# Optimization experiments

Measured on AMD Instinct MI355X. Metric: run time of the kernel, lower is better.

The kernel has to match this reference:

```python
import jax, jax.numpy as jnp
import numpy as np

HEADS = 8
DIM_HEAD = 64
SCALE = DIM_HEAD ** -0.5
QUERY_DIM = 512
CTX_DIM = 64
INNER = HEADS * DIM_HEAD  # 512
GATE_HID = 32


def setup_inputs() -> dict:
    key = jax.random.key(0)
    ks = jax.random.split(key, 11)
    B, N, M = 4, 2048, 2048
    s = lambda fan: 1.0 / np.sqrt(fan)
    return {
        "x": jax.random.normal(ks[0], (B, N, QUERY_DIM), dtype=jnp.float32),
        "context": jax.random.normal(ks[1], (B, M, CTX_DIM), dtype=jnp.float32),
        "Wq": jax.random.normal(ks[2], (QUERY_DIM, INNER), dtype=jnp.float32) * s(QUERY_DIM),
        "Wk": jax.random.normal(ks[3], (CTX_DIM, INNER), dtype=jnp.float32) * s(CTX_DIM),
        "Wv": jax.random.normal(ks[4], (CTX_DIM, INNER), dtype=jnp.float32) * s(CTX_DIM),
        "W1": jax.random.normal(ks[5], (CTX_DIM, GATE_HID), dtype=jnp.float32) * s(CTX_DIM),
        "b1": jnp.zeros((GATE_HID,), dtype=jnp.float32),
        "W2": jax.random.normal(ks[6], (GATE_HID, 1), dtype=jnp.float32) * s(GATE_HID),
        "b2": jnp.zeros((1,), dtype=jnp.float32),
        "Wo": jax.random.normal(ks[7], (INNER, QUERY_DIM), dtype=jnp.float32) * s(INNER),
        "bo": jnp.zeros((QUERY_DIM,), dtype=jnp.float32),
    }


def reference(x, context, Wq, Wk, Wv, W1, b1, W2, b2, Wo, bo):
    B, N, _ = x.shape
    M = context.shape[1]
    # visual reliability gate: sigmoid(relu(ctx @ W1 + b1) @ W2 + b2) -> [B, M, 1]
    gate = jax.nn.sigmoid(jax.nn.relu(context @ W1 + b1) @ W2 + b2)
    ctx = context * gate
    # projections
    q = (x @ Wq).reshape(B, N, HEADS, DIM_HEAD).transpose(0, 2, 1, 3)    # [B,H,N,D]
    k = (ctx @ Wk).reshape(B, M, HEADS, DIM_HEAD).transpose(0, 2, 1, 3)  # [B,H,M,D]
    v = (ctx @ Wv).reshape(B, M, HEADS, DIM_HEAD).transpose(0, 2, 1, 3)  # [B,H,M,D]
    # scaled dot-product attention (full score matrix, as in source)
    sim = jnp.einsum('bhid,bhjd->bhij', q, k) * SCALE
    attn = jax.nn.softmax(sim, axis=-1)
    out = jnp.einsum('bhij,bhjd->bhid', attn, v)
    out = out.transpose(0, 2, 1, 3).reshape(B, N, INNER)
    return out @ Wo + bo
```

## Files before the change

### kernel.cpp

```cpp
#include <hip/hip_runtime.h>

typedef unsigned short u16;
typedef unsigned int u32;
using frag16 = __attribute__((ext_vector_type(8))) short;
using facc   = __attribute__((ext_vector_type(4))) float;
using facc16 = __attribute__((ext_vector_type(16))) float;

#define DEV static __device__ __forceinline__

DEV u16 f2bf(float f) {
  union { float f; unsigned u; } v; v.f = f;
  unsigned r = v.u + 0x7fffu + ((v.u >> 16) & 1u);
  return (u16)(r >> 16);
}
DEV unsigned fbits(float f) {
  union { float f; unsigned u; } v; v.f = f;
  return v.u;
}
DEV unsigned pkbf(float lo, float hi) {
  return __builtin_amdgcn_perm(fbits(hi) + 0x8000u, fbits(lo) + 0x8000u, 0x07060302u);
}
DEV unsigned pkbf_t(float lo, float hi) {
  return __builtin_amdgcn_perm(fbits(hi), fbits(lo), 0x07060302u);
}
DEV void gld16(const u16* g, u16* l) {
  __builtin_amdgcn_global_load_lds(
      (__attribute__((address_space(1))) unsigned int*)(g),
      (__attribute__((address_space(3))) unsigned int*)(l), 16, 0, 0);
}

__global__ __launch_bounds__(256) void prep_gate_kernel(const float4* __restrict__ x,
    const float* __restrict__ Wq, const float* __restrict__ Wk,
    const float* __restrict__ Wv, const float* __restrict__ Wo,
    const float* __restrict__ ctx, const float* __restrict__ W1,
    const float* __restrict__ b1, const float* __restrict__ W2,
    const float* __restrict__ b2,
    u16* __restrict__ xb, u16* __restrict__ WqT, u16* __restrict__ WkT,
    u16* __restrict__ WvT, u16* __restrict__ WoT, u16* __restrict__ gctx) {
  int bid = blockIdx.x;
  if (bid < 4096) {
    int id = bid * 256 + threadIdx.x;
    float4 v = x[id];
    ushort4 o;
    o.x = f2bf(v.x); o.y = f2bf(v.y); o.z = f2bf(v.z); o.w = f2bf(v.w);
    *(ushort4*)(xb + (size_t)id * 4) = o;
  } else if (bid < 4240) {
    int job = bid - 4096;
    const float* W; u16* WT; int K, tile;
    if (job < 64)      { W = Wq; WT = WqT; K = 512; tile = job; }
    else if (job < 72) { W = Wk; WT = WkT; K = 64;  tile = job - 64; }
    else if (job < 80) { W = Wv; WT = WvT; K = 64;  tile = job - 72; }
    else               { W = Wo; WT = WoT; K = 512; tile = job - 80; }
    int tilesK = K >> 6;
    int tr = tile % tilesK, tc = tile / tilesK;
    __shared__ float tl[64][65];
    int c = threadIdx.x & 63, r4 = threadIdx.x >> 6;
    #pragma unroll
    for (int it = 0; it < 16; ++it) {
      int kk = it * 4 + r4;
      tl[kk][c] = W[(size_t)(tr * 64 + kk) * 512 + tc * 64 + c];
    }
    __syncthreads();
    #pragma unroll
    for (int it = 0; it < 16; ++it) {
      int nn = it * 4 + r4;
      WT[(size_t)(tc * 64 + nn) * K + tr * 64 + c] = f2bf(tl[c][nn]);
    }
  } else {
    int wave = threadIdx.x >> 6, lane = threadIdx.x & 63;
    int row = (bid - 4240) * 4 + wave;
    __shared__ float sc[4][64];
    float cv = ctx[(size_t)row * 64 + lane];
    sc[wave][lane] = cv;
    __syncthreads();
    float h = 0.f;
    if (lane < 32) {
      h = b1[lane];
      #pragma unroll
      for (int i = 0; i < 64; ++i) h += sc[wave][i] * W1[i * 32 + lane];
      h = fmaxf(h, 0.f) * W2[lane];
    }
    #pragma unroll
    for (int off = 32; off; off >>= 1) h += __shfl_xor(h, off);
    float g = 1.f / (1.f + __expf(-(h + b2[0])));
    gctx[(size_t)row * 64 + lane] = f2bf(cv * g);
  }
}

template<int MODE>
DEV void gemm128_body(const u16* __restrict__ A, const u16* __restrict__ BT,
                      void* __restrict__ Cp, const float* __restrict__ bias,
                      int m0, int n0, float scale,
                      u16* As0, u16* As1, u16* Bs0, u16* Bs1) {
  const int K = 512, N = 512;
  const int lane = threadIdx.x & 63, wave = threadIdx.x >> 6;
  const int quad = lane >> 4, l16 = lane & 15;
  const int wr = wave >> 1, wc = wave & 1;

  const u16* gA = A + (size_t)(m0 + wave * 32 + (lane >> 2)) * K + (lane & 3) * 8;
  const u16* gB = BT + (size_t)(n0 + wave * 16 + (lane >> 2)) * K + (lane & 3) * 8;

  facc acc[4][2] = {};

  for (int k0 = 0; k0 < K; k0 += 64) {
    if (k0) __syncthreads();
    gld16(gA + k0,           As0 + wave * 1024);
    gld16(gA + 16 * K + k0,  As0 + wave * 1024 + 512);
    gld16(gA + k0 + 32,          As1 + wave * 1024);
    gld16(gA + 16 * K + k0 + 32, As1 + wave * 1024 + 512);
    gld16(gB + k0,      Bs0 + wave * 512);
    gld16(gB + k0 + 32, Bs1 + wave * 512);
    __syncthreads();

    #pragma unroll
    for (int hh = 0; hh < 2; ++hh) {
      const u16* Ah = hh ? As1 : As0;
      const u16* Bh = hh ? Bs1 : Bs0;
      frag16 af[4], bf[2];
      #pragma unroll
      for (int rt = 0; rt < 4; ++rt)
        af[rt] = *(const frag16*)(Ah + (wr * 64 + rt * 16 + l16) * 32 + quad * 8);
      #pragma unroll
      for (int ct = 0; ct < 2; ++ct)
        bf[ct] = *(const frag16*)(Bh + (wc * 32 + ct * 16 + l16) * 32 + quad * 8);
      #pragma unroll
      for (int rt = 0; rt < 4; ++rt)
        #pragma unroll
        for (int ct = 0; ct < 2; ++ct)
          acc[rt][ct] = __builtin_amdgcn_mfma_f32_16x16x32_bf16(af[rt], bf[ct], acc[rt][ct], 0, 0, 0);
    }
  }

  #pragma unroll
  for (int rt = 0; rt < 4; ++rt) {
    #pragma unroll
    for (int ct = 0; ct < 2; ++ct) {
      int col = n0 + wc * 32 + ct * 16 + l16;
      int r0g = m0 + wr * 64 + rt * 16 + quad * 4;
      if (MODE == 0) {
        u16* C = (u16*)Cp;
        #pragma unroll
        for (int r = 0; r < 4; ++r)
          C[(size_t)(r0g + r) * N + col] = f2bf(acc[rt][ct][r] * scale);
      } else {
        float* C = (float*)Cp;
        float bv = bias[col];
        #pragma unroll
        for (int r = 0; r < 4; ++r)
          C[(size_t)(r0g + r) * N + col] = acc[rt][ct][r] + bv;
      }
    }
  }
}

__global__ __launch_bounds__(256) void proj_kernel(const u16* __restrict__ xb,
    const u16* __restrict__ WqT, u16* __restrict__ qb,
    const u16* __restrict__ gctx, const u16* __restrict__ BkT,
    const u16* __restrict__ BvT, u16* __restrict__ Kp, u16* __restrict__ Vp) {
  __shared__ __align__(16) u16 As0[128 * 32], As1[128 * 32];
  __shared__ __align__(16) u16 Bs0[64 * 32], Bs1[64 * 32];
  int bid = blockIdx.x;
  if (bid < 512) {
    int n0 = (bid & 7) * 64, m0 = (bid >> 3) * 128;
    gemm128_body<0>(xb, WqT, qb, nullptr, m0, n0,
                    0.125f * 1.4426950408889634f, As0, As1, Bs0, Bs1);
    return;
  }
  bid -= 512;
  const int Kd = 64;
  int lane = threadIdx.x & 63, wave = threadIdx.x >> 6;
  int quad = lane >> 4, l16 = lane & 15;
  int wr = wave >> 1, wc = wave & 1;
  int rowBase = (bid >> 3) * 64 + wr * 32;
  int colBase = (bid & 7) * 64 + wc * 32;
  facc ak[2][2] = {}, av[2][2] = {};
  const u16* a0 = gctx + (size_t)(rowBase + l16) * Kd + quad * 8;
  const u16* a1 = a0 + (size_t)16 * Kd;
  const u16* bk0 = BkT + (size_t)(colBase + l16) * Kd + quad * 8;
  const u16* bk1 = bk0 + (size_t)16 * Kd;
  const u16* bv0 = BvT + (size_t)(colBase + l16) * Kd + quad * 8;
  const u16* bv1 = bv0 + (size_t)16 * Kd;
  #pragma unroll
  for (int kk = 0; kk < Kd; kk += 32) {
    frag16 af0 = *(const frag16*)(a0 + kk);
    frag16 af1 = *(const frag16*)(a1 + kk);
    frag16 k0 = *(const frag16*)(bk0 + kk);
    frag16 k1 = *(const frag16*)(bk1 + kk);
    frag16 v0 = *(const frag16*)(bv0 + kk);
    frag16 v1 = *(const frag16*)(bv1 + kk);
    ak[0][0] = __builtin_amdgcn_mfma_f32_16x16x32_bf16(af0, k0, ak[0][0], 0, 0, 0);
    ak[0][1] = __builtin_amdgcn_mfma_f32_16x16x32_bf16(af0, k1, ak[0][1], 0, 0, 0);
    ak[1][0] = __builtin_amdgcn_mfma_f32_16x16x32_bf16(af1, k0, ak[1][0], 0, 0, 0);
    ak[1][1] = __builtin_amdgcn_mfma_f32_16x16x32_bf16(af1, k1, ak[1][1], 0, 0, 0);
    av[0][0] = __builtin_amdgcn_mfma_f32_16x16x32_bf16(af0, v0, av[0][0], 0, 0, 0);
    av[0][1] = __builtin_amdgcn_mfma_f32_16x16x32_bf16(af0, v1, av[0][1], 0, 0, 0);
    av[1][0] = __builtin_amdgcn_mfma_f32_16x16x32_bf16(af1, v0, av[1][0], 0, 0, 0);
    av[1][1] = __builtin_amdgcn_mfma_f32_16x16x32_bf16(af1, v1, av[1][1], 0, 0, 0);
  }
  #pragma unroll
  for (int rt = 0; rt < 2; ++rt) {
    #pragma unroll
    for (int ct = 0; ct < 2; ++ct) {
      int col = colBase + ct * 16 + l16;
      int r0g = rowBase + rt * 16 + quad * 4;
      int hh = col >> 6, d = col & 63;
      int b = r0g >> 11;
      #pragma unroll
      for (int r = 0; r < 4; ++r) {
        int m = (r0g + r) & 2047;
        size_t addr = ((((size_t)(b * 8 + hh) * 64 + (m >> 5)) * 4 + (d >> 4)) * 64
                       + ((d >> 3) & 1) * 32 + (m & 31)) * 8 + (d & 7);
        Kp[addr] = f2bf(ak[rt][ct][r]);
      }
      int m = r0g & 2047;
      size_t addr = ((((size_t)(b * 8 + hh) * 64 + (m >> 5)) * 4
                      + ((m >> 4) & 1) * 2 + (d >> 5)) * 64
                     + ((m >> 3) & 1) * 32 + (d & 31)) * 8 + (m & 7);
      ushort4 o;
      o.x = f2bf(av[rt][ct][0]); o.y = f2bf(av[rt][ct][1]);
      o.z = f2bf(av[rt][ct][2]); o.w = f2bf(av[rt][ct][3]);
      *(ushort4*)(Vp + addr) = o;
    }
  }
}

__global__ __launch_bounds__(256, 2) void attn_kernel(
    const u16* __restrict__ qb, const u16* __restrict__ Kp,
    const u16* __restrict__ Vp, u16* __restrict__ ob) {
  const int lane = threadIdx.x & 63, wave = threadIdx.x >> 6;
  const int l32 = lane & 31;
  const int hi = lane >> 5;
  const int bid = blockIdx.x;
  const int bh = bid & 31;
  const int qblk = bid >> 5;
  const int b = bh >> 3, h = bh & 7;
  const int q0 = (qblk * 4 + wave) * 32;
  const int rowg = b * 2048 + q0 + l32;

  __shared__ __align__(16) u16 sK[3][2][2048], sV[3][2][2048];

  const u16* qp = qb + (size_t)rowg * 512 + h * 64 + hi * 8;
  frag16 qf0 = *(const frag16*)(qp);
  frag16 qf1 = *(const frag16*)(qp + 16);
  frag16 qf2 = *(const frag16*)(qp + 32);
  frag16 qf3 = *(const frag16*)(qp + 48);

  frag16 ones;
  #pragma unroll
  for (int i = 0; i < 8; ++i) ones[i] = (short)0x3F80;

  facc16 O0 = {}, O1 = {}, Lacc = {};

  const size_t ts = 2048;
  const u16* kpb = Kp + (size_t)(bh * 64) * ts + wave * 512 + lane * 8;
  const u16* vpb = Vp + (size_t)(bh * 64) * ts + wave * 512 + lane * 8;

  auto STAGE = [&](int g, int buf) {
    const size_t t2 = (size_t)(2 * g) * ts;
    gld16(kpb + t2,      &sK[buf][0][0] + wave * 512);
    gld16(kpb + t2 + ts, &sK[buf][1][0] + wave * 512);
    gld16(vpb + t2,      &sV[buf][0][0] + wave * 512);
    gld16(vpb + t2 + ts, &sV[buf][1][0] + wave * 512);
  };

  STAGE(0, 0);
  STAGE(1, 1);

  int p = 0;
  #pragma unroll 1
  for (int g = 0; g < 32; ++g) {
    if (g < 31) {
      asm volatile("s_waitcnt vmcnt(4) lgkmcnt(0)" ::: "memory");
    } else {
      asm volatile("s_waitcnt vmcnt(0) lgkmcnt(0)" ::: "memory");
    }
    __builtin_amdgcn_s_barrier();

    const u16* kbase = &sK[p][0][0];
    const u16* vbase = &sV[p][0][0];

    frag16 kfa[4], kfb[4];
    #pragma unroll
    for (int i = 0; i < 4; ++i) {
      kfa[i] = *(const frag16*)(kbase + i * 512 + lane * 8);
      kfb[i] = *(const frag16*)(kbase + 2048 + i * 512 + lane * 8);
    }

    if (g + 2 < 32) {
      int ps = p + 2; if (ps >= 3) ps -= 3;
      STAGE(g + 2, ps);
    }

    facc16 Sa = {}, Sb = {};
    Sa = __builtin_amdgcn_mfma_f32_32x32x16_bf16(kfa[0], qf0, Sa, 0, 0, 0);
    Sb = __builtin_amdgcn_mfma_f32_32x32x16_bf16(kfb[0], qf0, Sb, 0, 0, 0);
    Sa = __builtin_amdgcn_mfma_f32_32x32x16_bf16(kfa[1], qf1, Sa, 0, 0, 0);
    Sb = __builtin_amdgcn_mfma_f32_32x32x16_bf16(kfb[1], qf1, Sb, 0, 0, 0);
    Sa = __builtin_amdgcn_mfma_f32_32x32x16_bf16(kfa[2], qf2, Sa, 0, 0, 0);
    Sb = __builtin_amdgcn_mfma_f32_32x32x16_bf16(kfb[2], qf2, Sb, 0, 0, 0);
    Sa = __builtin_amdgcn_mfma_f32_32x32x16_bf16(kfa[3], qf3, Sa, 0, 0, 0);
    Sb = __builtin_amdgcn_mfma_f32_32x32x16_bf16(kfb[3], qf3, Sb, 0, 0, 0);

    float ea[16], eb[16];
    #pragma unroll
    for (int r = 0; r < 16; ++r) { ea[r] = __builtin_amdgcn_exp2f(Sa[r]);
                                   eb[r] = __builtin_amdgcn_exp2f(Sb[r]); }

    unsigned pua[2][4], pub[2][4];
    #pragma unroll
    for (int c = 0; c < 2; ++c) {
      {
        const float* ee = ea + c * 8;
        unsigned L0 = pkbf_t(ee[0], ee[1]);
        unsigned L1 = pkbf_t(ee[2], ee[3]);
        unsigned H0 = pkbf_t(ee[4], ee[5]);
        unsigned H1 = pkbf_t(ee[6], ee[7]);
        unsigned Y0 = hi ? L0 : H0;
        unsigned Y1 = hi ? L1 : H1;
        unsigned X0 = (unsigned)__shfl_xor((int)Y0, 32);
        unsigned X1 = (unsigned)__shfl_xor((int)Y1, 32);
        pua[c][0] = hi ? X0 : L0;
        pua[c][1] = hi ? X1 : L1;
        pua[c][2] = hi ? H0 : X0;
        pua[c][3] = hi ? H1 : X1;
      }
      {
        const float* ee = eb + c * 8;
        unsigned L0 = pkbf_t(ee[0], ee[1]);
        unsigned L1 = pkbf_t(ee[2], ee[3]);
        unsigned H0 = pkbf_t(ee[4], ee[5]);
        unsigned H1 = pkbf_t(ee[6], ee[7]);
        unsigned Y0 = hi ? L0 : H0;
        unsigned Y1 = hi ? L1 : H1;
        unsigned X0 = (unsigned)__shfl_xor((int)Y0, 32);
        unsigned X1 = (unsigned)__shfl_xor((int)Y1, 32);
        pub[c][0] = hi ? X0 : L0;
        pub[c][1] = hi ? X1 : L1;
        pub[c][2] = hi ? H0 : X0;
        pub[c][3] = hi ? H1 : X1;
      }
    }
    frag16 Pa0 = *(frag16*)&pua[0][0];
    frag16 Pa1 = *(frag16*)&pua[1][0];
    frag16 Pb0 = *(frag16*)&pub[0][0];
    frag16 Pb1 = *(frag16*)&pub[1][0];

    Lacc = __builtin_amdgcn_mfma_f32_32x32x16_bf16(ones, Pa0, Lacc, 0, 0, 0);
    Lacc = __builtin_amdgcn_mfma_f32_32x32x16_bf16(ones, Pa1, Lacc, 0, 0, 0);
    Lacc = __builtin_amdgcn_mfma_f32_32x32x16_bf16(ones, Pb0, Lacc, 0, 0, 0);
    Lacc = __builtin_amdgcn_mfma_f32_32x32x16_bf16(ones, Pb1, Lacc, 0, 0, 0);

    frag16 vfa[4], vfb[4];
    #pragma unroll
    for (int i = 0; i < 4; ++i) {
      vfa[i] = *(const frag16*)(vbase + i * 512 + lane * 8);
      vfb[i] = *(const frag16*)(vbase + 2048 + i * 512 + lane * 8);
    }

    O0 = __builtin_amdgcn_mfma_f32_32x32x16_bf16(vfa[0], Pa0, O0, 0, 0, 0);
    O1 = __builtin_amdgcn_mfma_f32_32x32x16_bf16(vfa[1], Pa0, O1, 0, 0, 0);
    O0 = __builtin_amdgcn_mfma_f32_32x32x16_bf16(vfa[2], Pa1, O0, 0, 0, 0);
    O1 = __builtin_amdgcn_mfma_f32_32x32x16_bf16(vfa[3], Pa1, O1, 0, 0, 0);
    O0 = __builtin_amdgcn_mfma_f32_32x32x16_bf16(vfb[0], Pb0, O0, 0, 0, 0);
    O1 = __builtin_amdgcn_mfma_f32_32x32x16_bf16(vfb[1], Pb0, O1, 0, 0, 0);
    O0 = __builtin_amdgcn_mfma_f32_32x32x16_bf16(vfb[2], Pb1, O0, 0, 0, 0);
    O1 = __builtin_amdgcn_mfma_f32_32x32x16_bf16(vfb[3], Pb1, O1, 0, 0, 0);

    ++p; if (p == 3) p = 0;
  }

  float rinv = 1.0f / Lacc[0];

  u16* op = ob + (size_t)rowg * 512 + h * 64;
  #pragma unroll
  for (int dt = 0; dt < 2; ++dt) {
    #pragma unroll
    for (int rq = 0; rq < 4; ++rq) {
      float v0e, v1e, v2e, v3e;
      if (dt == 0) { v0e = O0[rq*4]; v1e = O0[rq*4+1]; v2e = O0[rq*4+2]; v3e = O0[rq*4+3]; }
      else         { v0e = O1[rq*4]; v1e = O1[rq*4+1]; v2e = O1[rq*4+2]; v3e = O1[rq*4+3]; }
      uint2 pk;
      pk.x = pkbf(v0e * rinv, v1e * rinv);
      pk.y = pkbf(v2e * rinv, v3e * rinv);
      int d0 = dt * 32 + 8 * rq + 4 * hi;
      *(uint2*)(op + d0) = pk;
    }
  }
}

__global__ __launch_bounds__(256) void gemm_out(const u16* __restrict__ A,
    const u16* __restrict__ BT, float* __restrict__ C,
    const float* __restrict__ bias) {
  __shared__ __align__(16) u16 As0[128 * 32], As1[128 * 32];
  __shared__ __align__(16) u16 Bs0[64 * 32], Bs1[64 * 32];
  int n0 = (blockIdx.x & 7) * 64, m0 = (blockIdx.x >> 3) * 128;
  gemm128_body<2>(A, BT, C, bias, m0, n0, 1.f, As0, As1, Bs0, Bs1);
}

extern "C" void kernel_launch(void* const* d_in, const int* in_sizes, int n_in,
                              void* d_out, int out_size, void* d_ws, size_t ws_size,
                              hipStream_t stream) {
  const float* x   = (const float*)d_in[0];
  const float* ctx = (const float*)d_in[1];
  const float* Wq  = (const float*)d_in[2];
  const float* Wk  = (const float*)d_in[3];
  const float* Wv  = (const float*)d_in[4];
  const float* W1  = (const float*)d_in[5];
  const float* b1  = (const float*)d_in[6];
  const float* W2  = (const float*)d_in[7];
  const float* b2  = (const float*)d_in[8];
  const float* Wo  = (const float*)d_in[9];
  const float* bo  = (const float*)d_in[10];
  float* out = (float*)d_out;

  char* ws = (char*)d_ws;
  size_t off = 0;
  auto alloc = [&](size_t bytes) {
    char* p = ws + off;
    off += (bytes + 255) & ~(size_t)255;
    return p;
  };
  u16* xb    = (u16*)alloc(8192ull * 512 * 2);
  u16* qb    = (u16*)alloc(8192ull * 512 * 2);
  u16* Kp    = (u16*)alloc(8192ull * 512 * 2);
  u16* Vp    = (u16*)alloc(8192ull * 512 * 2);
  u16* ob    = (u16*)alloc(8192ull * 512 * 2);
  u16* gctx  = (u16*)alloc(8192ull * 64 * 2);
  u16* WqT   = (u16*)alloc(512ull * 512 * 2);
  u16* WkT   = (u16*)alloc(512ull * 64 * 2);
  u16* WvT   = (u16*)alloc(512ull * 64 * 2);
  u16* WoT   = (u16*)alloc(512ull * 512 * 2);

  prep_gate_kernel<<<6288, 256, 0, stream>>>((const float4*)x, Wq, Wk, Wv, Wo,
                                             ctx, W1, b1, W2, b2,
                                             xb, WqT, WkT, WvT, WoT, gctx);
  proj_kernel<<<1536, 256, 0, stream>>>(xb, WqT, qb, gctx, WkT, WvT, Kp, Vp);
  attn_kernel<<<512, 256, 0, stream>>>(qb, Kp, Vp, ob);
  gemm_out<<<512, 256, 0, stream>>>(ob, WoT, out, bo);
}
```

Measured before the change: 168.5 us.

## Split attention keys across wave pairs and merge partial results in LDS

Each block now handles 64 queries. Two waves per query tile each process half of the key positions, and their partial O and row sums are combined through shared memory at the end. The grid doubles to 1024 blocks, launch bounds target 4 blocks per CU, and the K/V pipeline drops from triple to double buffering with a __syncthreads per iteration. This raises parallelism and occupancy but loads K/V tiles once per two query tiles instead of four, adds a reduction step, and gives the pipeline less prefetch depth.

```diff
diff --git a/kernel.cpp b/kernel.cpp
--- a/kernel.cpp
+++ b/kernel.cpp
@@ -224,20 +224,22 @@
   }
 }
 
-__global__ __launch_bounds__(256, 2) void attn_kernel(
+__global__ __launch_bounds__(256, 4) void attn_kernel(
     const u16* __restrict__ qb, const u16* __restrict__ Kp,
     const u16* __restrict__ Vp, u16* __restrict__ ob) {
   const int lane = threadIdx.x & 63, wave = threadIdx.x >> 6;
+  const int wq = wave & 1;
+  const int ws = wave >> 1;
   const int l32 = lane & 31;
   const int hi = lane >> 5;
   const int bid = blockIdx.x;
   const int bh = bid & 31;
-  const int qblk = bid >> 5;
+  const int qpair = bid >> 5;
   const int b = bh >> 3, h = bh & 7;
-  const int q0 = (qblk * 4 + wave) * 32;
+  const int q0 = qpair * 64 + wq * 32;
   const int rowg = b * 2048 + q0 + l32;
 
-  __shared__ __align__(16) u16 sK[3][2][2048], sV[3][2][2048];
+  __shared__ __align__(16) u16 sK[2][2][2048], sV[2][2][2048];
 
   const u16* qp = qb + (size_t)rowg * 512 + h * 64 + hi * 8;
   frag16 qf0 = *(const frag16*)(qp);
@@ -252,138 +254,113 @@
   facc16 O0 = {}, O1 = {}, Lacc = {};
 
   const size_t ts = 2048;
-  const u16* kpb = Kp + (size_t)(bh * 64) * ts + wave * 512 + lane * 8;
-  const u16* vpb = Vp + (size_t)(bh * 64) * ts + wave * 512 + lane * 8;
+  const u16* kpb = Kp + (size_t)(bh * 64 + ws * 32) * ts + wq * 1024 + lane * 8;
+  const u16* vpb = Vp + (size_t)(bh * 64 + ws * 32) * ts + wq * 1024 + lane * 8;
 
   auto STAGE = [&](int g, int buf) {
-    const size_t t2 = (size_t)(2 * g) * ts;
-    gld16(kpb + t2,      &sK[buf][0][0] + wave * 512);
-    gld16(kpb + t2 + ts, &sK[buf][1][0] + wave * 512);
-    gld16(vpb + t2,      &sV[buf][0][0] + wave * 512);
-    gld16(vpb + t2 + ts, &sV[buf][1][0] + wave * 512);
+    const size_t off = (size_t)g * ts;
+    gld16(kpb + off,       &sK[buf][ws][0] + wq * 1024);
+    gld16(kpb + off + 512, &sK[buf][ws][0] + wq * 1024 + 512);
+    gld16(vpb + off,       &sV[buf][ws][0] + wq * 1024);
+    gld16(vpb + off + 512, &sV[buf][ws][0] + wq * 1024 + 512);
   };
 
   STAGE(0, 0);
-  STAGE(1, 1);
 
   int p = 0;
   #pragma unroll 1
   for (int g = 0; g < 32; ++g) {
-    if (g < 31) {
-      asm volatile("s_waitcnt vmcnt(4) lgkmcnt(0)" ::: "memory");
-    } else {
-      asm volatile("s_waitcnt vmcnt(0) lgkmcnt(0)" ::: "memory");
-    }
-    __builtin_amdgcn_s_barrier();
-
-    const u16* kbase = &sK[p][0][0];
-    const u16* vbase = &sV[p][0][0];
-
-    frag16 kfa[4], kfb[4];
-    #pragma unroll
-    for (int i = 0; i < 4; ++i) {
-      kfa[i] = *(const frag16*)(kbase + i * 512 + lane * 8);
-      kfb[i] = *(const frag16*)(kbase + 2048 + i * 512 + lane * 8);
-    }
-
-    if (g + 2 < 32) {
-      int ps = p + 2; if (ps >= 3) ps -= 3;
-      STAGE(g + 2, ps);
-    }
-
-    facc16 Sa = {}, Sb = {};
-    Sa = __builtin_amdgcn_mfma_f32_32x32x16_bf16(kfa[0], qf0, Sa, 0, 0, 0);
-    Sb = __builtin_amdgcn_mfma_f32_32x32x16_bf16(kfb[0], qf0, Sb, 0, 0, 0);
-    Sa = __builtin_amdgcn_mfma_f32_32x32x16_bf16(kfa[1], qf1, Sa, 0, 0, 0);
-    Sb = __builtin_amdgcn_mfma_f32_32x32x16_bf16(kfb[1], qf1, Sb, 0, 0, 0);
-    Sa = __builtin_amdgcn_mfma_f32_32x32x16_bf16(kfa[2], qf2, Sa, 0, 0, 0);
-    Sb = __builtin_amdgcn_mfma_f32_32x32x16_bf16(kfb[2], qf2, Sb, 0, 0, 0);
-    Sa = __builtin_amdgcn_mfma_f32_32x32x16_bf16(kfa[3], qf3, Sa, 0, 0, 0);
-    Sb = __builtin_amdgcn_mfma_f32_32x32x16_bf16(kfb[3], qf3, Sb, 0, 0, 0);
-
-    float ea[16], eb[16];
-    #pragma unroll
-    for (int r = 0; r < 16; ++r) { ea[r] = __builtin_amdgcn_exp2f(Sa[r]);
-                                   eb[r] = __builtin_amdgcn_exp2f(Sb[r]); }
-
-    unsigned pua[2][4], pub[2][4];
+    __syncthreads();
+    if (g + 1 < 32) STAGE(g + 1, p ^ 1);
+
+    const u16* kbase = &sK[p][ws][0];
+    const u16* vbase = &sV[p][ws][0];
+
+    frag16 kf0 = *(const frag16*)(kbase + 0 * 512 + lane * 8);
+    frag16 kf1 = *(const frag16*)(kbase + 1 * 512 + lane * 8);
+    frag16 kf2 = *(const frag16*)(kbase + 2 * 512 + lane * 8);
+    frag16 kf3 = *(const frag16*)(kbase + 3 * 512 + lane * 8);
+
+    facc16 Sa = {};
+    Sa = __builtin_amdgcn_mfma_f32_32x32x16_bf16(kf0, qf0, Sa, 0, 0, 0);
+    Sa = __builtin_amdgcn_mfma_f32_32x32x16_bf16(kf1, qf1, Sa, 0, 0, 0);
+    Sa = __builtin_amdgcn_mfma_f32_32x32x16_bf16(kf2, qf2, Sa, 0, 0, 0);
+    Sa = __builtin_amdgcn_mfma_f32_32x32x16_bf16(kf3, qf3, Sa, 0, 0, 0);
+
+    float ea[16];
+    #pragma unroll
+    for (int r = 0; r < 16; ++r) ea[r] = __builtin_amdgcn_exp2f(Sa[r]);
+
+    unsigned pua[2][4];
     #pragma unroll
     for (int c = 0; c < 2; ++c) {
-      {
-        const float* ee = ea + c * 8;
-        unsigned L0 = pkbf_t(ee[0], ee[1]);
-        unsigned L1 = pkbf_t(ee[2], ee[3]);
-        unsigned H0 = pkbf_t(ee[4], ee[5]);
-        unsigned H1 = pkbf_t(ee[6], ee[7]);
-        unsigned Y0 = hi ? L0 : H0;
-        unsigned Y1 = hi ? L1 : H1;
-        unsigned X0 = (unsigned)__shfl_xor((int)Y0, 32);
-        unsigned X1 = (unsigned)__shfl_xor((int)Y1, 32);
-        pua[c][0] = hi ? X0 : L0;
-        pua[c][1] = hi ? X1 : L1;
-        pua[c][2] = hi ? H0 : X0;
-        pua[c][3] = hi ? H1 : X1;
-      }
-      {
-        const float* ee = eb + c * 8;
-        unsigned L0 = pkbf_t(ee[0], ee[1]);
-        unsigned L1 = pkbf_t(ee[2], ee[3]);
-        unsigned H0 = pkbf_t(ee[4], ee[5]);
-        unsigned H1 = pkbf_t(ee[6], ee[7]);
-        unsigned Y0 = hi ? L0 : H0;
-        unsigned Y1 = hi ? L1 : H1;
-        unsigned X0 = (unsigned)__shfl_xor((int)Y0, 32);
-        unsigned X1 = (unsigned)__shfl_xor((int)Y1, 32);
-        pub[c][0] = hi ? X0 : L0;
-        pub[c][1] = hi ? X1 : L1;
-        pub[c][2] = hi ? H0 : X0;
-        pub[c][3] = hi ? H1 : X1;
-      }
+      const float* ee = ea + c * 8;
+      unsigned L0 = pkbf_t(ee[0], ee[1]);
+      unsigned L1 = pkbf_t(ee[2], ee[3]);
+      unsigned H0 = pkbf_t(ee[4], ee[5]);
+      unsigned H1 = pkbf_t(ee[6], ee[7]);
+      unsigned Y0 = hi ? L0 : H0;
+      unsigned Y1 = hi ? L1 : H1;
+      unsigned X0 = (unsigned)__shfl_xor((int)Y0, 32);
+      unsigned X1 = (unsigned)__shfl_xor((int)Y1, 32);
+      pua[c][0] = hi ? X0 : L0;
+      pua[c][1] = hi ? X1 : L1;
+      pua[c][2] = hi ? H0 : X0;
+      pua[c][3] = hi ? H1 : X1;
     }
     frag16 Pa0 = *(frag16*)&pua[0][0];
     frag16 Pa1 = *(frag16*)&pua[1][0];
-    frag16 Pb0 = *(frag16*)&pub[0][0];
-    frag16 Pb1 = *(frag16*)&pub[1][0];
 
     Lacc = __builtin_amdgcn_mfma_f32_32x32x16_bf16(ones, Pa0, Lacc, 0, 0, 0);
     Lacc = __builtin_amdgcn_mfma_f32_32x32x16_bf16(ones, Pa1, Lacc, 0, 0, 0);
-    Lacc = __builtin_amdgcn_mfma_f32_32x32x16_bf16(ones, Pb0, Lacc, 0, 0, 0);
-    Lacc = __builtin_amdgcn_mfma_f32_32x32x16_bf16(ones, Pb1, Lacc, 0, 0, 0);
-
-    frag16 vfa[4], vfb[4];
-    #pragma unroll
-    for (int i = 0; i < 4; ++i) {
-      vfa[i] = *(const frag16*)(vbase + i * 512 + lane * 8);
-      vfb[i] = *(const frag16*)(vbase + 2048 + i * 512 + lane * 8);
-    }
-
-    O0 = __builtin_amdgcn_mfma_f32_32x32x16_bf16(vfa[0], Pa0, O0, 0, 0, 0);
-    O1 = __builtin_amdgcn_mfma_f32_32x32x16_bf16(vfa[1], Pa0, O1, 0, 0, 0);
-    O0 = __builtin_amdgcn_mfma_f32_32x32x16_bf16(vfa[2], Pa1, O0, 0, 0, 0);
-    O1 = __builtin_amdgcn_mfma_f32_32x32x16_bf16(vfa[3], Pa1, O1, 0, 0, 0);
-    O0 = __builtin_amdgcn_mfma_f32_32x32x16_bf16(vfb[0], Pb0, O0, 0, 0, 0);
-    O1 = __builtin_amdgcn_mfma_f32_32x32x16_bf16(vfb[1], Pb0, O1, 0, 0, 0);
-    O0 = __builtin_amdgcn_mfma_f32_32x32x16_bf16(vfb[2], Pb1, O0, 0, 0, 0);
-    O1 = __builtin_amdgcn_mfma_f32_32x32x16_bf16(vfb[3], Pb1, O1, 0, 0, 0);
-
-    ++p; if (p == 3) p = 0;
-  }
-
-  float rinv = 1.0f / Lacc[0];
-
-  u16* op = ob + (size_t)rowg * 512 + h * 64;
-  #pragma unroll
-  for (int dt = 0; dt < 2; ++dt) {
-    #pragma unroll
-    for (int rq = 0; rq < 4; ++rq) {
-      float v0e, v1e, v2e, v3e;
-      if (dt == 0) { v0e = O0[rq*4]; v1e = O0[rq*4+1]; v2e = O0[rq*4+2]; v3e = O0[rq*4+3]; }
-      else         { v0e = O1[rq*4]; v1e = O1[rq*4+1]; v2e = O1[rq*4+2]; v3e = O1[rq*4+3]; }
-      uint2 pk;
-      pk.x = pkbf(v0e * rinv, v1e * rinv);
-      pk.y = pkbf(v2e * rinv, v3e * rinv);
-      int d0 = dt * 32 + 8 * rq + 4 * hi;
-      *(uint2*)(op + d0) = pk;
+
+    frag16 vf0 = *(const frag16*)(vbase + 0 * 512 + lane * 8);
+    frag16 vf1 = *(const frag16*)(vbase + 1 * 512 + lane * 8);
+    frag16 vf2 = *(const frag16*)(vbase + 2 * 512 + lane * 8);
+    frag16 vf3 = *(const frag16*)(vbase + 3 * 512 + lane * 8);
+
+    O0 = __builtin_amdgcn_mfma_f32_32x32x16_bf16(vf0, Pa0, O0, 0, 0, 0);
+    O1 = __builtin_amdgcn_mfma_f32_32x32x16_bf16(vf1, Pa0, O1, 0, 0, 0);
+    O0 = __builtin_amdgcn_mfma_f32_32x32x16_bf16(vf2, Pa1, O0, 0, 0, 0);
+    O1 = __builtin_amdgcn_mfma_f32_32x32x16_bf16(vf3, Pa1, O1, 0, 0, 0);
+
+    p ^= 1;
+  }
+
+  float* mO = (float*)&sK[0][0][0];
+  float* mL = (float*)&sV[0][0][0];
+  __syncthreads();
+  if (ws == 1) {
+    #pragma unroll
+    for (int r = 0; r < 16; ++r) {
+      mO[r * 128 + wq * 64 + lane]        = O0[r];
+      mO[(r + 16) * 128 + wq * 64 + lane] = O1[r];
+    }
+    mL[wq * 64 + lane] = Lacc[0];
+  }
+  __syncthreads();
+  if (ws == 0) {
+    #pragma unroll
+    for (int r = 0; r < 16; ++r) {
+      O0[r] += mO[r * 128 + wq * 64 + lane];
+      O1[r] += mO[(r + 16) * 128 + wq * 64 + lane];
+    }
+    float rinv = 1.0f / (Lacc[0] + mL[wq * 64 + lane]);
+
+    u16* op = ob + (size_t)rowg * 512 + h * 64;
+    #pragma unroll
+    for (int dt = 0; dt < 2; ++dt) {
+      #pragma unroll
+      for (int rq = 0; rq < 4; ++rq) {
+        float v0e, v1e, v2e, v3e;
+        if (dt == 0) { v0e = O0[rq*4]; v1e = O0[rq*4+1]; v2e = O0[rq*4+2]; v3e = O0[rq*4+3]; }
+        else         { v0e = O1[rq*4]; v1e = O1[rq*4+1]; v2e = O1[rq*4+2]; v3e = O1[rq*4+3]; }
+        uint2 pk;
+        pk.x = pkbf(v0e * rinv, v1e * rinv);
+        pk.y = pkbf(v2e * rinv, v3e * rinv);
+        int d0 = dt * 32 + 8 * rq + 4 * hi;
+        *(uint2*)(op + d0) = pk;
+      }
     }
   }
 }
@@ -435,6 +412,6 @@
                                              ctx, W1, b1, W2, b2,
                                              xb, WqT, WkT, WvT, WoT, gctx);
   proj_kernel<<<1536, 256, 0, stream>>>(xb, WqT, qb, gctx, WkT, WvT, Kp, Vp);
-  attn_kernel<<<512, 256, 0, stream>>>(qb, Kp, Vp, ob);
+  attn_kernel<<<1024, 256, 0, stream>>>(qb, Kp, Vp, ob);
   gemm_out<<<512, 256, 0, stream>>>(ob, WoT, out, bo);
 }
```

Measured after the change: 174.1 us. +3.4%, slower.
